# Kernel optimization log

Hardware: AMD Instinct MI355X
Metric: run time of the kernel (lower is better)

Reference implementation:

```python
import jax, jax.numpy as jnp
import numpy as np

N, T, K, V, E = 64, 256, 64, 32000, 100


def setup_inputs() -> dict:
    key = jax.random.key(0)
    ks = jax.random.split(key, 7)
    x = jax.random.randint(ks[0], (N, T), 0, V)
    emb_weight = jax.random.normal(ks[1], (V, E), dtype=jnp.float32)
    # trans: Linear(E, K*K, bias=False), weight uniform(-1,1)
    W_trans = jax.random.uniform(ks[2], (K * K, E), minval=-1.0, maxval=1.0, dtype=jnp.float32)
    # start: Linear(1, K)
    start_w = jax.random.normal(ks[3], (K, 1), dtype=jnp.float32) * 0.1
    start_b = jax.random.normal(ks[4], (K,), dtype=jnp.float32) * 0.1
    # emb_cluster: Embedding(K, K)
    emb_cluster_w = jax.random.normal(ks[5], (K, K), dtype=jnp.float32)
    # vocab: Linear(K, V, bias=False), weight uniform(-1,1)
    vocab_w = jax.random.uniform(ks[6], (V, K), minval=-1.0, maxval=1.0, dtype=jnp.float32)
    return {"x": x, "emb_weight": emb_weight, "W_trans": W_trans,
            "start_w": start_w, "start_b": start_b,
            "emb_cluster_w": emb_cluster_w, "vocab_w": vocab_w}


def reference(x, emb_weight, W_trans, start_w, start_b, emb_cluster_w, vocab_w):
    n, t = x.shape
    k = emb_cluster_w.shape[0]
    # word embeddings used to condition transitions at steps 0..T-2
    xe = emb_weight[x[:, :-1]]                                   # [N,T-1,E]
    # transition log-probs: log_softmax over destination state
    tran = jax.nn.log_softmax(
        jnp.einsum('nte,ce->ntc', xe, W_trans).reshape(n, t - 1, k, k), axis=-1)
    # emission log-probs per cluster: E[k, v]
    Elog = jax.nn.log_softmax(emb_cluster_w @ vocab_w.T, axis=-1)  # [K,V]
    emit = Elog.T[x[:, 1:]]                                       # [N,T-1,K]
    # initial alpha: log_softmax(start(ones)) expanded over batch
    alpha0 = jax.nn.log_softmax(start_w[:, 0] + start_b)           # [K]
    alpha0 = jnp.broadcast_to(alpha0[None, :], (n, k))
    tran_t = jnp.moveaxis(tran, 1, 0)   # [T-1,N,K,K]
    emit_t = jnp.moveaxis(emit, 1, 0)   # [T-1,N,K]

    def step(alpha, te):
        tr, em = te
        # logsumexp over previous state j: alpha[n,j] + tr[n,j,k]
        a = jax.scipy.special.logsumexp(alpha[:, :, None] + tr, axis=1) + em
        return a, None

    alpha, _ = jax.lax.scan(step, alpha0, (tran_t, emit_t))
    return -jnp.mean(jax.scipy.special.logsumexp(alpha, axis=1))
```

## Files before the change

kernel.cpp:

```cpp
#include <hip/hip_runtime.h>
#include <hip/hip_bf16.h>
#include <stdint.h>

#define NT 16320
#define NTPAD 16384
#define KDIM 128
#define NCOLS 4096
#define NSEQ 64
#define TSTEPS 255
#define VOCAB 32000
#define EDIM 100
#define CHUNKS 17
#define CLEN 15

typedef __attribute__((ext_vector_type(8))) short s8v;
typedef __attribute__((ext_vector_type(4))) float f4v;

__device__ __forceinline__ float bflo(uint32_t u) { return __uint_as_float(u << 16); }
__device__ __forceinline__ float bfhi(uint32_t u) { return __uint_as_float(u & 0xffff0000u); }

__device__ __forceinline__ void load_lds16(const void* g, void* l) {
    __builtin_amdgcn_global_load_lds(
        (const __attribute__((address_space(1))) void*)(uintptr_t)g,
        (__attribute__((address_space(3))) void*)(uintptr_t)l,
        16, 0, 0);
}

__global__ __launch_bounds__(256) void prep_ab(const int* __restrict__ x,
                                               const float* __restrict__ emb,
                                               const float* __restrict__ Wt,
                                               __hip_bfloat16* __restrict__ A,
                                               __hip_bfloat16* __restrict__ B) {
    int tid = threadIdx.x;
    int rloc = tid >> 4, q = tid & 15;
    int b = blockIdx.x * 16 + rloc;
    int c0 = q * 8;
    float vals[8] = {0.f, 0.f, 0.f, 0.f, 0.f, 0.f, 0.f, 0.f};
    __hip_bfloat16* dst;
    if (b < NTPAD) {
        if (b < NT) {
            int n = b / TSTEPS;
            int t = b - n * TSTEPS;
            int tok = x[n * 256 + t];
            const float* er = emb + (size_t)tok * EDIM;
#pragma unroll
            for (int i = 0; i < 8; ++i) { int e = c0 + i; if (e < EDIM) vals[i] = er[e]; }
        }
        dst = A + (size_t)b * KDIM + c0;
    } else {
        int cc = b - NTPAD;
        const float* wr = Wt + (size_t)cc * EDIM;
#pragma unroll
        for (int i = 0; i < 8; ++i) { int e = c0 + i; if (e < EDIM) vals[i] = wr[e]; }
        dst = B + (size_t)cc * KDIM + c0;
    }
    union { __hip_bfloat16 h[8]; uint4 u; } pk;
#pragma unroll
    for (int i = 0; i < 8; ++i) pk.h[i] = __float2bfloat16(vals[i]);
    *(uint4*)dst = pk.u;
}

__global__ __launch_bounds__(256) void gemm_kern(const __hip_bfloat16* __restrict__ A,
                                                 const __hip_bfloat16* __restrict__ B,
                                                 const __hip_bfloat16* __restrict__ emB,
                                                 __hip_bfloat16* __restrict__ Eg) {
    int mblk = blockIdx.x;
    int nblk = blockIdx.y;
    int tid = threadIdx.x, wave = tid >> 6, lane = tid & 63;

    __shared__ __align__(16) char smem[65536];
    char* sA = smem;
    char* sB = smem + 32768;

    {
        int r0 = wave * 32;
        int l16 = lane & 15;
        int rsub = lane >> 4;
#pragma unroll
        for (int g = 0; g < 8; ++g) {
            int r = r0 + g * 4 + rsub;
            int chunk = l16 ^ (r & 7);
            const char* gp = (const char*)(A + (size_t)(mblk * 128 + r) * KDIM) + chunk * 16;
            load_lds16(gp, sA + (r0 + g * 4) * 256);
        }
#pragma unroll
        for (int g = 0; g < 8; ++g) {
            int c = r0 + g * 4 + rsub;
            int chunk = l16 ^ (c & 7);
            const char* gp = (const char*)(B + (size_t)(nblk * 128 + c) * KDIM) + chunk * 16;
            load_lds16(gp, sB + (r0 + g * 4) * 256);
        }
    }
    __syncthreads();

    int wc = (wave >> 1) * 64, wm = (wave & 1) * 64;
    int l15 = lane & 15, g4 = lane >> 4;
    f4v acc[4][4] = {};
#pragma unroll
    for (int k32 = 0; k32 < 4; ++k32) {
        s8v af[4], bf[4];
#pragma unroll
        for (int jt = 0; jt < 4; ++jt) {
            int r = wc + jt * 16 + l15;
            int chunk = (k32 * 4 + g4) ^ (r & 7);
            af[jt] = *(const s8v*)(sB + r * 256 + chunk * 16);
        }
#pragma unroll
        for (int mt = 0; mt < 4; ++mt) {
            int r = wm + mt * 16 + l15;
            int chunk = (k32 * 4 + g4) ^ (r & 7);
            bf[mt] = *(const s8v*)(sA + r * 256 + chunk * 16);
        }
#pragma unroll
        for (int jt = 0; jt < 4; ++jt)
#pragma unroll
            for (int mt = 0; mt < 4; ++mt)
                acc[jt][mt] = __builtin_amdgcn_mfma_f32_16x16x32_bf16(af[jt], bf[mt], acc[jt][mt], 0, 0, 0);
    }
    __syncthreads();

    char* sW = smem;
    const char* emb8 = (const char*)emB;
#pragma unroll
    for (int mt = 0; mt < 4; ++mt) {
        int mrow = wm + mt * 16 + l15;
        int mglob = mblk * 128 + mrow;
        float v[16];
#pragma unroll
        for (int jt = 0; jt < 4; ++jt)
#pragma unroll
            for (int rr = 0; rr < 4; ++rr) v[jt * 4 + rr] = acc[jt][mt][rr];
        float mx = v[0];
#pragma unroll
        for (int k = 1; k < 16; ++k) mx = fmaxf(mx, v[k]);
        mx = fmaxf(mx, __shfl_xor(mx, 16, 64));
        mx = fmaxf(mx, __shfl_xor(mx, 32, 64));
        float ex[16], sg = 0.f;
#pragma unroll
        for (int k = 0; k < 16; ++k) { ex[k] = __expf(v[k] - mx); sg += ex[k]; }
        sg += __shfl_xor(sg, 16, 64);
        sg += __shfl_xor(sg, 32, 64);
        float inv = 1.0f / sg;
        uint4 e0 = *(const uint4*)(emb8 + (size_t)mglob * 128 + g4 * 32);
        uint4 e1 = *(const uint4*)(emb8 + (size_t)mglob * 128 + g4 * 32 + 16);
        float em[16];
        {
            const uint32_t* w0 = (const uint32_t*)&e0;
            const uint32_t* w1 = (const uint32_t*)&e1;
#pragma unroll
            for (int i = 0; i < 4; ++i) {
                em[2 * i] = bflo(w0[i]);     em[2 * i + 1] = bfhi(w0[i]);
                em[8 + 2 * i] = bflo(w1[i]); em[8 + 2 * i + 1] = bfhi(w1[i]);
            }
        }
#pragma unroll
        for (int jt = 0; jt < 4; ++jt) {
            union { __hip_bfloat16 h[4]; uint2 u; } pk;
#pragma unroll
            for (int rr = 0; rr < 4; ++rr)
                pk.h[rr] = __float2bfloat16(ex[jt * 4 + rr] * inv * em[jt * 4 + rr]);
            *(uint2*)(sW + mrow * 272 + (wc + jt * 16 + g4 * 4) * 2) = pk.u;
        }
    }
    __syncthreads();

    {
        int rloc = tid >> 3;
        int q = tid & 7;
#pragma unroll
        for (int rp = 0; rp < 4; ++rp) {
            int row = rp * 32 + rloc;
            char* dst = (char*)Eg + (size_t)(mblk * 128 + row) * 8192 + nblk * 256;
            const char* src = sW + row * 272;
            *(uint4*)(dst + q * 16)       = *(const uint4*)(src + q * 16);
            *(uint4*)(dst + 128 + q * 16) = *(const uint4*)(src + 128 + q * 16);
        }
    }
}

__global__ __launch_bounds__(256) void dkern(const float* __restrict__ ec,
                                             const float* __restrict__ vw,
                                             float* __restrict__ partials) {
    int tid = threadIdx.x;
    int wave = tid >> 6, lane = tid & 63;
    float er[64];
    {
        const float4* ecv = (const float4*)(ec + (size_t)lane * 64);
#pragma unroll
        for (int i = 0; i < 16; ++i) {
            float4 v = ecv[i];
            er[4 * i] = v.x; er[4 * i + 1] = v.y; er[4 * i + 2] = v.z; er[4 * i + 3] = v.w;
        }
    }
    int v0 = blockIdx.x * 125;
    float m = -1e30f, s = 0.f;
    for (int v = v0 + wave; v < v0 + 125; v += 4) {
        int vu = __builtin_amdgcn_readfirstlane(v);
        const float* row = vw + (size_t)vu * 64;
        float acc = 0.f;
#pragma unroll
        for (int e = 0; e < 64; ++e) acc += er[e] * row[e];
        float nm = fmaxf(m, acc);
        s = s * __expf(m - nm) + __expf(acc - nm);
        m = nm;
    }
    __shared__ float pm[4][64], ps[4][64];
    pm[wave][lane] = m; ps[wave][lane] = s;
    __syncthreads();
    if (tid < 64) {
        float M = pm[0][tid], Ssum = ps[0][tid];
#pragma unroll
        for (int w = 1; w < 4; ++w) {
            float m2 = pm[w][tid], s2 = ps[w][tid];
            float nm = fmaxf(M, m2);
            Ssum = Ssum * __expf(M - nm) + s2 * __expf(m2 - nm);
            M = nm;
        }
        partials[(blockIdx.x * 64 + tid) * 2]     = M;
        partials[(blockIdx.x * 64 + tid) * 2 + 1] = Ssum;
    }
}

__global__ __launch_bounds__(256) void dreduce(const float* __restrict__ partials,
                                               float* __restrict__ d) {
    __shared__ float pm[4][64], ps[4][64];
    int k = threadIdx.x & 63, part = threadIdx.x >> 6;
    float M = -1e30f, S = 0.f;
    for (int b = part; b < 256; b += 4) {
        float m2 = partials[(b * 64 + k) * 2];
        float s2 = partials[(b * 64 + k) * 2 + 1];
        float nm = fmaxf(M, m2);
        S = S * __expf(M - nm) + s2 * __expf(m2 - nm);
        M = nm;
    }
    pm[part][k] = M; ps[part][k] = S;
    __syncthreads();
    if (threadIdx.x < 64) {
        float Mm = pm[0][k], Ss = ps[0][k];
#pragma unroll
        for (int w = 1; w < 4; ++w) {
            float m2 = pm[w][k], s2 = ps[w][k];
            float nm = fmaxf(Mm, m2);
            Ss = Ss * __expf(Mm - nm) + s2 * __expf(m2 - nm);
            Mm = nm;
        }
        d[k] = Mm + __logf(Ss);
    }
}

__global__ __launch_bounds__(256) void emit_kern(const int* __restrict__ x,
                                                 const float* __restrict__ ec,
                                                 const float* __restrict__ vw,
                                                 const float* __restrict__ d,
                                                 __hip_bfloat16* __restrict__ emB) {
    int tid = threadIdx.x;
    int wave = tid >> 6, lane = tid & 63;
    float er[64];
    {
        const float4* ecv = (const float4*)(ec + (size_t)lane * 64);
#pragma unroll
        for (int i = 0; i < 16; ++i) {
            float4 v = ecv[i];
            er[4 * i] = v.x; er[4 * i + 1] = v.y; er[4 * i + 2] = v.z; er[4 * i + 3] = v.w;
        }
    }
    float dj = d[lane];
    int j = lane;
    int pos = ((j >> 2) & 3) * 16 + ((j >> 4) & 3) * 4 + (j & 3);
    int nt0 = blockIdx.x * 16 + wave * 4;
#pragma unroll
    for (int s = 0; s < 4; ++s) {
        int nt = nt0 + s;
        int n = nt / TSTEPS;
        int t = nt - n * TSTEPS;
        int tok = x[n * 256 + t + 1];
        tok = __builtin_amdgcn_readfirstlane(tok);
        const float* row = vw + (size_t)tok * 64;
        float acc = 0.f;
#pragma unroll
        for (int e = 0; e < 64; ++e) acc += er[e] * row[e];
        emB[(size_t)nt * 64 + pos] = __float2bfloat16(__expf(acc - dj));
    }
}

__global__ __launch_bounds__(64) void chunk_kern(const __hip_bfloat16* __restrict__ Eg,
                                                 __hip_bfloat16* __restrict__ Gout,
                                                 float* __restrict__ Rout) {
    int lane = threadIdx.x;
    int l15 = lane & 15, g4 = lane >> 4;
    int id = blockIdx.x;
    int n = (id * 3856) >> 16;
    int c = id - n * 17;
    int base_m = n * TSTEPS + c * CLEN;

    __shared__ __align__(16) char sGT[64 * 144];

    {
        uint4 z = {0, 0, 0, 0};
#pragma unroll
        for (int i = 0; i < 8; ++i) *(uint4*)(sGT + lane * 144 + i * 16) = z;
        *(uint16_t*)(sGT + lane * 144 + lane * 2) = 0x3F80;
    }

    const char* Ebase = (const char*)Eg;
    uint4 pf[4][2];
    {
        const char* tp = Ebase + (size_t)(base_m + 14) * 8192;
#pragma unroll
        for (int at = 0; at < 4; ++at)
#pragma unroll
            for (int kk = 0; kk < 2; ++kk)
                pf[at][kk] = *(const uint4*)(tp + (at * 16 + l15) * 128 + kk * 64 + g4 * 16);
    }

    float rlog[4] = {0.f, 0.f, 0.f, 0.f};

    for (int tl = 14; tl >= 0; --tl) {
        uint4 af[4][2];
#pragma unroll
        for (int at = 0; at < 4; ++at) { af[at][0] = pf[at][0]; af[at][1] = pf[at][1]; }
        if (tl > 0) {
            const char* tp = Ebase + (size_t)(base_m + tl - 1) * 8192;
#pragma unroll
            for (int at = 0; at < 4; ++at)
#pragma unroll
                for (int kk = 0; kk < 2; ++kk)
                    pf[at][kk] = *(const uint4*)(tp + (at * 16 + l15) * 128 + kk * 64 + g4 * 16);
        }

        f4v acc[4][4] = {};
#pragma unroll
        for (int kk = 0; kk < 2; ++kk) {
#pragma unroll
            for (int ct = 0; ct < 4; ++ct) {
                s8v b = *(const s8v*)(sGT + (ct * 16 + l15) * 144 + kk * 64 + g4 * 16);
#pragma unroll
                for (int at = 0; at < 4; ++at)
                    acc[at][ct] = __builtin_amdgcn_mfma_f32_16x16x32_bf16(
                        *(const s8v*)&af[at][kk], b, acc[at][ct], 0, 0, 0);
            }
        }

#pragma unroll
        for (int ct = 0; ct < 4; ++ct) {
            float mx = acc[0][ct][0];
#pragma unroll
            for (int at = 0; at < 4; ++at)
#pragma unroll
                for (int rr = 0; rr < 4; ++rr) mx = fmaxf(mx, acc[at][ct][rr]);
            mx = fmaxf(mx, __shfl_xor(mx, 16, 64));
            mx = fmaxf(mx, __shfl_xor(mx, 32, 64));
            mx = fmaxf(mx, 1e-38f);
            rlog[ct] += __logf(mx);
            float inv = 1.0f / mx;
            int col = ct * 16 + l15;
#pragma unroll
            for (int at = 0; at < 4; ++at) {
                union { __hip_bfloat16 h[4]; uint2 u; } pk;
#pragma unroll
                for (int rr = 0; rr < 4; ++rr)
                    pk.h[rr] = __float2bfloat16(acc[at][ct][rr] * inv);
                *(uint2*)(sGT + col * 144 + at * 32 + g4 * 8) = pk.u;
            }
        }
    }

    {
        char* go = (char*)(Gout + (size_t)id * 4096 + lane * 64);
#pragma unroll
        for (int i = 0; i < 8; ++i)
            *(uint4*)(go + i * 16) = *(const uint4*)(sGT + lane * 144 + i * 16);
    }
    if (g4 == 0)
#pragma unroll
        for (int ct = 0; ct < 4; ++ct)
            Rout[(size_t)id * 64 + ct * 16 + l15] = rlog[ct];
}

__global__ __launch_bounds__(64) void combine_kern(const __hip_bfloat16* __restrict__ G,
                                                   const float* __restrict__ R,
                                                   const float* __restrict__ sw,
                                                   const float* __restrict__ sb,
                                                   float* __restrict__ out) {
    int n = blockIdx.x;
    int lane = threadIdx.x;
    __shared__ __align__(16) float sV[64];

    float alpha;
    {
        float v = sw[lane] + sb[lane];
        float m = v;
#pragma unroll
        for (int off = 1; off < 64; off <<= 1) m = fmaxf(m, __shfl_xor(m, off, 64));
        float s = __expf(v - m);
#pragma unroll
        for (int off = 1; off < 64; off <<= 1) s += __shfl_xor(s, off, 64);
        alpha = v - (m + __logf(s));
    }

    const char* Gb = (const char*)(G + (size_t)n * CHUNKS * 4096) + lane * 128;
    const float* Rb = R + (size_t)n * CHUNKS * 64 + lane;

    uint4 pf[8];
#pragma unroll
    for (int i = 0; i < 8; ++i) pf[i] = *(const uint4*)(Gb + i * 16);
    float rpf = Rb[0];

    for (int c = 0; c < CHUNKS; ++c) {
        uint4 cur[8];
#pragma unroll
        for (int i = 0; i < 8; ++i) cur[i] = pf[i];
        float rc = rpf;
        if (c + 1 < CHUNKS) {
            const char* gn = Gb + (size_t)(c + 1) * 8192;
#pragma unroll
            for (int i = 0; i < 8; ++i) pf[i] = *(const uint4*)(gn + i * 16);
            rpf = Rb[(c + 1) * 64];
        }

        float m = alpha;
#pragma unroll
        for (int off = 1; off < 64; off <<= 1) m = fmaxf(m, __shfl_xor(m, off, 64));
        sV[lane] = __expf(alpha - m);
        float acc = 0.f;
        const float4* sv4 = (const float4*)sV;
#pragma unroll
        for (int i = 0; i < 8; ++i) {
            const uint32_t* gw = (const uint32_t*)&cur[i];
            float4 va = sv4[2 * i], vb = sv4[2 * i + 1];
            acc += va.x * bflo(gw[0]) + va.y * bfhi(gw[0]);
            acc += va.z * bflo(gw[1]) + va.w * bfhi(gw[1]);
            acc += vb.x * bflo(gw[2]) + vb.y * bfhi(gw[2]);
            acc += vb.z * bflo(gw[3]) + vb.w * bfhi(gw[3]);
        }
        alpha = m + __logf(fmaxf(acc, 1e-38f)) + rc;
    }

    {
        float m = alpha;
#pragma unroll
        for (int off = 1; off < 64; off <<= 1) m = fmaxf(m, __shfl_xor(m, off, 64));
        float s = __expf(alpha - m);
#pragma unroll
        for (int off = 1; off < 64; off <<= 1) s += __shfl_xor(s, off, 64);
        if (lane == 0) atomicAdd(out, -(m + __logf(s)) * (1.0f / 64.0f));
    }
}

extern "C" void kernel_launch(void* const* d_in, const int* in_sizes, int n_in,
                              void* d_out, int out_size, void* d_ws, size_t ws_size,
                              hipStream_t stream) {
    const int*   x   = (const int*)d_in[0];
    const float* emb = (const float*)d_in[1];
    const float* Wt  = (const float*)d_in[2];
    const float* sw  = (const float*)d_in[3];
    const float* sb  = (const float*)d_in[4];
    const float* ec  = (const float*)d_in[5];
    const float* vw  = (const float*)d_in[6];
    float* out = (float*)d_out;
    char* ws = (char*)d_ws;

    __hip_bfloat16* Eg  = (__hip_bfloat16*)ws;
    __hip_bfloat16* A   = (__hip_bfloat16*)(ws + 134217728ull);
    __hip_bfloat16* B   = (__hip_bfloat16*)(ws + 138412032ull);
    __hip_bfloat16* emB = (__hip_bfloat16*)(ws + 139460608ull);
    float* dvec         = (float*)(ws + 141557760ull);
    float* partials     = (float*)(ws + 141558784ull);
    __hip_bfloat16* Gc  = (__hip_bfloat16*)(ws + 141689856ull);
    float* Rc           = (float*)(ws + 150602752ull);

    hipMemsetAsync(out, 0, sizeof(float), stream);

    prep_ab<<<(NTPAD + NCOLS) / 16, 256, 0, stream>>>(x, emb, Wt, A, B);
    dkern<<<256, 256, 0, stream>>>(ec, vw, partials);
    dreduce<<<1, 256, 0, stream>>>(partials, dvec);
    emit_kern<<<NT / 16, 256, 0, stream>>>(x, ec, vw, dvec, emB);
    gemm_kern<<<dim3(NTPAD / 128, NCOLS / 128), 256, 0, stream>>>(A, B, emB, Eg);
    chunk_kern<<<NSEQ * CHUNKS, 64, 0, stream>>>(Eg, Gc, Rc);
    combine_kern<<<NSEQ, 64, 0, stream>>>(Gc, Rc, sw, sb, out);
}
```

Before: 224.1 us.

## Merge prep and normalizer kernels; split chunked scan into 32 shorter chunks

Fuses the A/B bf16 packing kernel and the emission-normalizer partial kernel into one launch, with block ranges dispatching to each role. This removes one kernel launch and lets the two independent jobs run concurrently. It also changes the chunked forward scan from 17 chunks of 15 steps to 32 chunks of 8 steps, giving more parallel blocks and a shorter serial chain per block. The cost is more partial products for the combine stage to multiply. The Gc/Rc workspace is relocated to reuse the A/B region, which is safe because gemm_kern has finished reading A/B before chunk_kern writes Gc.

```diff
diff --git a/kernel.cpp b/kernel.cpp
--- a/kernel.cpp
+++ b/kernel.cpp
@@ -10,8 +10,8 @@
 #define TSTEPS 255
 #define VOCAB 32000
 #define EDIM 100
-#define CHUNKS 17
-#define CLEN 15
+#define CHUNKS 32
+#define CLEN 8
 
 typedef __attribute__((ext_vector_type(8))) short s8v;
 typedef __attribute__((ext_vector_type(4))) float f4v;
@@ -26,198 +26,82 @@
         16, 0, 0);
 }
 
-__global__ __launch_bounds__(256) void prep_ab(const int* __restrict__ x,
+__global__ __launch_bounds__(256) void prep_dk(const int* __restrict__ x,
                                                const float* __restrict__ emb,
                                                const float* __restrict__ Wt,
+                                               const float* __restrict__ ec,
+                                               const float* __restrict__ vw,
                                                __hip_bfloat16* __restrict__ A,
-                                               __hip_bfloat16* __restrict__ B) {
+                                               __hip_bfloat16* __restrict__ B,
+                                               float* __restrict__ partials) {
+    int bid = blockIdx.x;
     int tid = threadIdx.x;
-    int rloc = tid >> 4, q = tid & 15;
-    int b = blockIdx.x * 16 + rloc;
-    int c0 = q * 8;
-    float vals[8] = {0.f, 0.f, 0.f, 0.f, 0.f, 0.f, 0.f, 0.f};
-    __hip_bfloat16* dst;
-    if (b < NTPAD) {
-        if (b < NT) {
-            int n = b / TSTEPS;
-            int t = b - n * TSTEPS;
-            int tok = x[n * 256 + t];
-            const float* er = emb + (size_t)tok * EDIM;
-#pragma unroll
-            for (int i = 0; i < 8; ++i) { int e = c0 + i; if (e < EDIM) vals[i] = er[e]; }
-        }
-        dst = A + (size_t)b * KDIM + c0;
+    if (bid < 1280) {
+        int rloc = tid >> 4, q = tid & 15;
+        int b = bid * 16 + rloc;
+        int c0 = q * 8;
+        float vals[8] = {0.f, 0.f, 0.f, 0.f, 0.f, 0.f, 0.f, 0.f};
+        __hip_bfloat16* dst;
+        if (b < NTPAD) {
+            if (b < NT) {
+                int n = b / TSTEPS;
+                int t = b - n * TSTEPS;
+                int tok = x[n * 256 + t];
+                const float* er = emb + (size_t)tok * EDIM;
+#pragma unroll
+                for (int i = 0; i < 8; ++i) { int e = c0 + i; if (e < EDIM) vals[i] = er[e]; }
+            }
+            dst = A + (size_t)b * KDIM + c0;
+        } else {
+            int cc = b - NTPAD;
+            const float* wr = Wt + (size_t)cc * EDIM;
+#pragma unroll
+            for (int i = 0; i < 8; ++i) { int e = c0 + i; if (e < EDIM) vals[i] = wr[e]; }
+            dst = B + (size_t)cc * KDIM + c0;
+        }
+        union { __hip_bfloat16 h[8]; uint4 u; } pk;
+#pragma unroll
+        for (int i = 0; i < 8; ++i) pk.h[i] = __float2bfloat16(vals[i]);
+        *(uint4*)dst = pk.u;
     } else {
-        int cc = b - NTPAD;
-        const float* wr = Wt + (size_t)cc * EDIM;
-#pragma unroll
-        for (int i = 0; i < 8; ++i) { int e = c0 + i; if (e < EDIM) vals[i] = wr[e]; }
-        dst = B + (size_t)cc * KDIM + c0;
-    }
-    union { __hip_bfloat16 h[8]; uint4 u; } pk;
-#pragma unroll
-    for (int i = 0; i < 8; ++i) pk.h[i] = __float2bfloat16(vals[i]);
-    *(uint4*)dst = pk.u;
-}
-
-__global__ __launch_bounds__(256) void gemm_kern(const __hip_bfloat16* __restrict__ A,
-                                                 const __hip_bfloat16* __restrict__ B,
-                                                 const __hip_bfloat16* __restrict__ emB,
-                                                 __hip_bfloat16* __restrict__ Eg) {
-    int mblk = blockIdx.x;
-    int nblk = blockIdx.y;
-    int tid = threadIdx.x, wave = tid >> 6, lane = tid & 63;
-
-    __shared__ __align__(16) char smem[65536];
-    char* sA = smem;
-    char* sB = smem + 32768;
-
-    {
-        int r0 = wave * 32;
-        int l16 = lane & 15;
-        int rsub = lane >> 4;
-#pragma unroll
-        for (int g = 0; g < 8; ++g) {
-            int r = r0 + g * 4 + rsub;
-            int chunk = l16 ^ (r & 7);
-            const char* gp = (const char*)(A + (size_t)(mblk * 128 + r) * KDIM) + chunk * 16;
-            load_lds16(gp, sA + (r0 + g * 4) * 256);
-        }
-#pragma unroll
-        for (int g = 0; g < 8; ++g) {
-            int c = r0 + g * 4 + rsub;
-            int chunk = l16 ^ (c & 7);
-            const char* gp = (const char*)(B + (size_t)(nblk * 128 + c) * KDIM) + chunk * 16;
-            load_lds16(gp, sB + (r0 + g * 4) * 256);
-        }
-    }
-    __syncthreads();
-
-    int wc = (wave >> 1) * 64, wm = (wave & 1) * 64;
-    int l15 = lane & 15, g4 = lane >> 4;
-    f4v acc[4][4] = {};
-#pragma unroll
-    for (int k32 = 0; k32 < 4; ++k32) {
-        s8v af[4], bf[4];
-#pragma unroll
-        for (int jt = 0; jt < 4; ++jt) {
-            int r = wc + jt * 16 + l15;
-            int chunk = (k32 * 4 + g4) ^ (r & 7);
-            af[jt] = *(const s8v*)(sB + r * 256 + chunk * 16);
-        }
-#pragma unroll
-        for (int mt = 0; mt < 4; ++mt) {
-            int r = wm + mt * 16 + l15;
-            int chunk = (k32 * 4 + g4) ^ (r & 7);
-            bf[mt] = *(const s8v*)(sA + r * 256 + chunk * 16);
-        }
-#pragma unroll
-        for (int jt = 0; jt < 4; ++jt)
-#pragma unroll
-            for (int mt = 0; mt < 4; ++mt)
-                acc[jt][mt] = __builtin_amdgcn_mfma_f32_16x16x32_bf16(af[jt], bf[mt], acc[jt][mt], 0, 0, 0);
-    }
-    __syncthreads();
-
-    char* sW = smem;
-    const char* emb8 = (const char*)emB;
-#pragma unroll
-    for (int mt = 0; mt < 4; ++mt) {
-        int mrow = wm + mt * 16 + l15;
-        int mglob = mblk * 128 + mrow;
-        float v[16];
-#pragma unroll
-        for (int jt = 0; jt < 4; ++jt)
-#pragma unroll
-            for (int rr = 0; rr < 4; ++rr) v[jt * 4 + rr] = acc[jt][mt][rr];
-        float mx = v[0];
-#pragma unroll
-        for (int k = 1; k < 16; ++k) mx = fmaxf(mx, v[k]);
-        mx = fmaxf(mx, __shfl_xor(mx, 16, 64));
-        mx = fmaxf(mx, __shfl_xor(mx, 32, 64));
-        float ex[16], sg = 0.f;
-#pragma unroll
-        for (int k = 0; k < 16; ++k) { ex[k] = __expf(v[k] - mx); sg += ex[k]; }
-        sg += __shfl_xor(sg, 16, 64);
-        sg += __shfl_xor(sg, 32, 64);
-        float inv = 1.0f / sg;
-        uint4 e0 = *(const uint4*)(emb8 + (size_t)mglob * 128 + g4 * 32);
-        uint4 e1 = *(const uint4*)(emb8 + (size_t)mglob * 128 + g4 * 32 + 16);
-        float em[16];
+        int db = bid - 1280;
+        int wave = tid >> 6, lane = tid & 63;
+        float er[64];
         {
-            const uint32_t* w0 = (const uint32_t*)&e0;
-            const uint32_t* w1 = (const uint32_t*)&e1;
-#pragma unroll
-            for (int i = 0; i < 4; ++i) {
-                em[2 * i] = bflo(w0[i]);     em[2 * i + 1] = bfhi(w0[i]);
-                em[8 + 2 * i] = bflo(w1[i]); em[8 + 2 * i + 1] = bfhi(w1[i]);
-            }
-        }
-#pragma unroll
-        for (int jt = 0; jt < 4; ++jt) {
-            union { __hip_bfloat16 h[4]; uint2 u; } pk;
-#pragma unroll
-            for (int rr = 0; rr < 4; ++rr)
-                pk.h[rr] = __float2bfloat16(ex[jt * 4 + rr] * inv * em[jt * 4 + rr]);
-            *(uint2*)(sW + mrow * 272 + (wc + jt * 16 + g4 * 4) * 2) = pk.u;
-        }
-    }
-    __syncthreads();
-
-    {
-        int rloc = tid >> 3;
-        int q = tid & 7;
-#pragma unroll
-        for (int rp = 0; rp < 4; ++rp) {
-            int row = rp * 32 + rloc;
-            char* dst = (char*)Eg + (size_t)(mblk * 128 + row) * 8192 + nblk * 256;
-            const char* src = sW + row * 272;
-            *(uint4*)(dst + q * 16)       = *(const uint4*)(src + q * 16);
-            *(uint4*)(dst + 128 + q * 16) = *(const uint4*)(src + 128 + q * 16);
-        }
-    }
-}
-
-__global__ __launch_bounds__(256) void dkern(const float* __restrict__ ec,
-                                             const float* __restrict__ vw,
-                                             float* __restrict__ partials) {
-    int tid = threadIdx.x;
-    int wave = tid >> 6, lane = tid & 63;
-    float er[64];
-    {
-        const float4* ecv = (const float4*)(ec + (size_t)lane * 64);
-#pragma unroll
-        for (int i = 0; i < 16; ++i) {
-            float4 v = ecv[i];
-            er[4 * i] = v.x; er[4 * i + 1] = v.y; er[4 * i + 2] = v.z; er[4 * i + 3] = v.w;
-        }
-    }
-    int v0 = blockIdx.x * 125;
-    float m = -1e30f, s = 0.f;
-    for (int v = v0 + wave; v < v0 + 125; v += 4) {
-        int vu = __builtin_amdgcn_readfirstlane(v);
-        const float* row = vw + (size_t)vu * 64;
-        float acc = 0.f;
-#pragma unroll
-        for (int e = 0; e < 64; ++e) acc += er[e] * row[e];
-        float nm = fmaxf(m, acc);
-        s = s * __expf(m - nm) + __expf(acc - nm);
-        m = nm;
-    }
-    __shared__ float pm[4][64], ps[4][64];
-    pm[wave][lane] = m; ps[wave][lane] = s;
-    __syncthreads();
-    if (tid < 64) {
-        float M = pm[0][tid], Ssum = ps[0][tid];
-#pragma unroll
-        for (int w = 1; w < 4; ++w) {
-            float m2 = pm[w][tid], s2 = ps[w][tid];
-            float nm = fmaxf(M, m2);
-            Ssum = Ssum * __expf(M - nm) + s2 * __expf(m2 - nm);
-            M = nm;
-        }
-        partials[(blockIdx.x * 64 + tid) * 2]     = M;
-        partials[(blockIdx.x * 64 + tid) * 2 + 1] = Ssum;
+            const float4* ecv = (const float4*)(ec + (size_t)lane * 64);
+#pragma unroll
+            for (int i = 0; i < 16; ++i) {
+                float4 v = ecv[i];
+                er[4 * i] = v.x; er[4 * i + 1] = v.y; er[4 * i + 2] = v.z; er[4 * i + 3] = v.w;
+            }
+        }
+        int v0 = db * 125;
+        float m = -1e30f, s = 0.f;
+        for (int v = v0 + wave; v < v0 + 125; v += 4) {
+            int vu = __builtin_amdgcn_readfirstlane(v);
+            const float* row = vw + (size_t)vu * 64;
+            float acc = 0.f;
+#pragma unroll
+            for (int e = 0; e < 64; ++e) acc += er[e] * row[e];
+            float nm = fmaxf(m, acc);
+            s = s * __expf(m - nm) + __expf(acc - nm);
+            m = nm;
+        }
+        __shared__ float pm[4][64], ps[4][64];
+        pm[wave][lane] = m; ps[wave][lane] = s;
+        __syncthreads();
+        if (tid < 64) {
+            float M = pm[0][tid], Ssum = ps[0][tid];
+#pragma unroll
+            for (int w = 1; w < 4; ++w) {
+                float m2 = pm[w][tid], s2 = ps[w][tid];
+                float nm = fmaxf(M, m2);
+                Ssum = Ssum * __expf(M - nm) + s2 * __expf(m2 - nm);
+                M = nm;
+            }
+            partials[(db * 64 + tid) * 2]     = M;
+            partials[(db * 64 + tid) * 2 + 1] = Ssum;
+        }
     }
 }
 
@@ -283,15 +167,134 @@
     }
 }
 
+__global__ __launch_bounds__(256) void gemm_kern(const __hip_bfloat16* __restrict__ A,
+                                                 const __hip_bfloat16* __restrict__ B,
+                                                 const __hip_bfloat16* __restrict__ emB,
+                                                 __hip_bfloat16* __restrict__ Eg) {
+    int mblk = blockIdx.x;
+    int nblk = blockIdx.y;
+    int tid = threadIdx.x, wave = tid >> 6, lane = tid & 63;
+
+    __shared__ __align__(16) char smem[65536];
+    char* sA = smem;
+    char* sB = smem + 32768;
+
+    {
+        int r0 = wave * 32;
+        int l16 = lane & 15;
+        int rsub = lane >> 4;
+#pragma unroll
+        for (int g = 0; g < 8; ++g) {
+            int r = r0 + g * 4 + rsub;
+            int chunk = l16 ^ (r & 7);
+            const char* gp = (const char*)(A + (size_t)(mblk * 128 + r) * KDIM) + chunk * 16;
+            load_lds16(gp, sA + (r0 + g * 4) * 256);
+        }
+#pragma unroll
+        for (int g = 0; g < 8; ++g) {
+            int c = r0 + g * 4 + rsub;
+            int chunk = l16 ^ (c & 7);
+            const char* gp = (const char*)(B + (size_t)(nblk * 128 + c) * KDIM) + chunk * 16;
+            load_lds16(gp, sB + (r0 + g * 4) * 256);
+        }
+    }
+    __syncthreads();
+
+    int wc = (wave >> 1) * 64, wm = (wave & 1) * 64;
+    int l15 = lane & 15, g4 = lane >> 4;
+    f4v acc[4][4] = {};
+#pragma unroll
+    for (int k32 = 0; k32 < 4; ++k32) {
+        s8v af[4], bf[4];
+#pragma unroll
+        for (int jt = 0; jt < 4; ++jt) {
+            int r = wc + jt * 16 + l15;
+            int chunk = (k32 * 4 + g4) ^ (r & 7);
+            af[jt] = *(const s8v*)(sB + r * 256 + chunk * 16);
+        }
+#pragma unroll
+        for (int mt = 0; mt < 4; ++mt) {
+            int r = wm + mt * 16 + l15;
+            int chunk = (k32 * 4 + g4) ^ (r & 7);
+            bf[mt] = *(const s8v*)(sA + r * 256 + chunk * 16);
+        }
+#pragma unroll
+        for (int jt = 0; jt < 4; ++jt)
+#pragma unroll
+            for (int mt = 0; mt < 4; ++mt)
+                acc[jt][mt] = __builtin_amdgcn_mfma_f32_16x16x32_bf16(af[jt], bf[mt], acc[jt][mt], 0, 0, 0);
+    }
+    __syncthreads();
+
+    char* sW = smem;
+    const char* emb8 = (const char*)emB;
+#pragma unroll
+    for (int mt = 0; mt < 4; ++mt) {
+        int mrow = wm + mt * 16 + l15;
+        int mglob = mblk * 128 + mrow;
+        float v[16];
+#pragma unroll
+        for (int jt = 0; jt < 4; ++jt)
+#pragma unroll
+            for (int rr = 0; rr < 4; ++rr) v[jt * 4 + rr] = acc[jt][mt][rr];
+        float mx = v[0];
+#pragma unroll
+        for (int k = 1; k < 16; ++k) mx = fmaxf(mx, v[k]);
+        mx = fmaxf(mx, __shfl_xor(mx, 16, 64));
+        mx = fmaxf(mx, __shfl_xor(mx, 32, 64));
+        float ex[16], sg = 0.f;
+#pragma unroll
+        for (int k = 0; k < 16; ++k) { ex[k] = __expf(v[k] - mx); sg += ex[k]; }
+        sg += __shfl_xor(sg, 16, 64);
+        sg += __shfl_xor(sg, 32, 64);
+        float inv = 1.0f / sg;
+        uint4 e0 = *(const uint4*)(emb8 + (size_t)mglob * 128 + g4 * 32);
+        uint4 e1 = *(const uint4*)(emb8 + (size_t)mglob * 128 + g4 * 32 + 16);
+        float em[16];
+        {
+            const uint32_t* w0 = (const uint32_t*)&e0;
+            const uint32_t* w1 = (const uint32_t*)&e1;
+#pragma unroll
+            for (int i = 0; i < 4; ++i) {
+                em[2 * i] = bflo(w0[i]);     em[2 * i + 1] = bfhi(w0[i]);
+                em[8 + 2 * i] = bflo(w1[i]); em[8 + 2 * i + 1] = bfhi(w1[i]);
+            }
+        }
+#pragma unroll
+        for (int jt = 0; jt < 4; ++jt) {
+            union { __hip_bfloat16 h[4]; uint2 u; } pk;
+#pragma unroll
+            for (int rr = 0; rr < 4; ++rr)
+                pk.h[rr] = __float2bfloat16(ex[jt * 4 + rr] * inv * em[jt * 4 + rr]);
+            *(uint2*)(sW + mrow * 272 + (wc + jt * 16 + g4 * 4) * 2) = pk.u;
+        }
+    }
+    __syncthreads();
+
+    {
+        int rloc = tid >> 3;
+        int q = tid & 7;
+#pragma unroll
+        for (int rp = 0; rp < 4; ++rp) {
+            int row = rp * 32 + rloc;
+            char* dst = (char*)Eg + (size_t)(mblk * 128 + row) * 8192 + nblk * 256;
+            const char* src = sW + row * 272;
+            *(uint4*)(dst + q * 16)       = *(const uint4*)(src + q * 16);
+            *(uint4*)(dst + 128 + q * 16) = *(const uint4*)(src + 128 + q * 16);
+        }
+    }
+}
+
 __global__ __launch_bounds__(64) void chunk_kern(const __hip_bfloat16* __restrict__ Eg,
                                                  __hip_bfloat16* __restrict__ Gout,
                                                  float* __restrict__ Rout) {
     int lane = threadIdx.x;
     int l15 = lane & 15, g4 = lane >> 4;
     int id = blockIdx.x;
-    int n = (id * 3856) >> 16;
-    int c = id - n * 17;
+    int n = id >> 5;
+    int c = id & 31;
     int base_m = n * TSTEPS + c * CLEN;
+    int len = (c == 31) ? 7 : 8;
 
     __shared__ __align__(16) char sGT[64 * 144];
 
@@ -305,7 +308,7 @@
     const char* Ebase = (const char*)Eg;
     uint4 pf[4][2];
     {
-        const char* tp = Ebase + (size_t)(base_m + 14) * 8192;
+        const char* tp = Ebase + (size_t)(base_m + len - 1) * 8192;
 #pragma unroll
         for (int at = 0; at < 4; ++at)
 #pragma unroll
@@ -315,7 +318,7 @@
 
     float rlog[4] = {0.f, 0.f, 0.f, 0.f};
 
-    for (int tl = 14; tl >= 0; --tl) {
+    for (int tl = len - 1; tl >= 0; --tl) {
         uint4 af[4][2];
 #pragma unroll
         for (int at = 0; at < 4; ++at) { af[at][0] = pf[at][0]; af[at][1] = pf[at][1]; }
@@ -466,13 +469,12 @@
     __hip_bfloat16* emB = (__hip_bfloat16*)(ws + 139460608ull);
     float* dvec         = (float*)(ws + 141557760ull);
     float* partials     = (float*)(ws + 141558784ull);
-    __hip_bfloat16* Gc  = (__hip_bfloat16*)(ws + 141689856ull);
-    float* Rc           = (float*)(ws + 150602752ull);
+    __hip_bfloat16* Gc  = (__hip_bfloat16*)(ws + 134217728ull);
+    float* Rc           = (float*)(ws + 150994944ull);
 
     hipMemsetAsync(out, 0, sizeof(float), stream);
 
-    prep_ab<<<(NTPAD + NCOLS) / 16, 256, 0, stream>>>(x, emb, Wt, A, B);
-    dkern<<<256, 256, 0, stream>>>(ec, vw, partials);
+    prep_dk<<<1536, 256, 0, stream>>>(x, emb, Wt, ec, vw, A, B, partials);
     dreduce<<<1, 256, 0, stream>>>(partials, dvec);
     emit_kern<<<NT / 16, 256, 0, stream>>>(x, ec, vw, dvec, emB);
     gemm_kern<<<dim3(NTPAD / 128, NCOLS / 128), 256, 0, stream>>>(A, B, emB, Eg);
```

New measurement: 231.0 us. +3.1%, slower.
